# Kernel tuning notes

Measured on AMD Instinct MI355X. Metric: run time of the kernel, lower is better.

The kernel has to match this reference:

```python
import jax, jax.numpy as jnp
import numpy as np

N_NODES = 100000


def gcn_conv(x, src, dst, W, b, n_nodes):
    """PyG GCNConv: out = D^{-1/2} (A + I) D^{-1/2} (x @ W) + b.
    src/dst are the original (non-self-loop) edges; self loops handled analytically.
    """
    h = x @ W  # [N, out]
    ones = jnp.ones(src.shape[0], dtype=h.dtype)
    # degree including self loop
    deg = jax.ops.segment_sum(ones, dst, num_segments=n_nodes) + 1.0  # [N]
    dinv = jax.lax.rsqrt(deg)
    norm = dinv[src] * dinv[dst]  # [E]
    msg = h[src] * norm[:, None]  # gather + scale
    agg = jax.ops.segment_sum(msg, dst, num_segments=n_nodes)  # scatter-add
    # self-loop contribution: norm = deg^{-1/2} * deg^{-1/2} = 1/deg
    agg = agg + h * (1.0 / deg)[:, None]
    return agg + b


def setup_inputs() -> dict:
    key = jax.random.key(0)
    k1, k2, k3, k4 = jax.random.split(key, 4)
    n, e = N_NODES, 3200000
    x = jax.random.normal(k1, (n, 256), dtype=jnp.float32)
    edge_index = jax.random.randint(k2, (2, e), 0, n, dtype=jnp.int64)
    W1 = jax.random.normal(k3, (256, 64), dtype=jnp.float32) * (1.0 / np.sqrt(256))
    b1 = jnp.zeros((64,), dtype=jnp.float32)
    W2 = jax.random.normal(k4, (64, 4), dtype=jnp.float32) * (1.0 / np.sqrt(64))
    b2 = jnp.zeros((4,), dtype=jnp.float32)
    return {"x": x, "edge_index": edge_index, "W1": W1, "b1": b1, "W2": W2, "b2": b2}


def reference(x, edge_index, W1, b1, W2, b2):
    n = x.shape[0]
    src, dst = edge_index[0], edge_index[1]
    h = gcn_conv(x, src, dst, W1, b1, n)
    h = jax.nn.leaky_relu(h, negative_slope=0.01)  # nn.LeakyReLU default
    # F.dropout in eval mode is identity
    h = gcn_conv(h, src, dst, W2, b2, n)
    return jax.nn.softmax(h, axis=1)
```

## Files before the change

kernel.cpp:

```cpp
#include <hip/hip_runtime.h>
#include <hip/hip_bf16.h>
#include <math.h>


#define NB 512
#define MAXB 512

typedef __attribute__((ext_vector_type(8))) short bf16x8;
typedef __attribute__((ext_vector_type(4))) float f32x4;

__device__ __forceinline__ int edge_val(const void* ep, size_t idx, int is64) {
    if (is64) return (int)(((const long long*)ep)[idx]);
    return ((const int*)ep)[idx];
}

__device__ __forceinline__ unsigned short f2bf(float f) {
    unsigned int u = __float_as_uint(f);
    return (unsigned short)((u + 0x7FFFu + ((u >> 16) & 1u)) >> 16);
}
__device__ __forceinline__ float bf2f(unsigned short b) {
    return __uint_as_float((unsigned int)b << 16);
}

__global__ void detect_width(const unsigned int* __restrict__ ew, int* __restrict__ flag) {
    if (threadIdx.x == 0 && blockIdx.x == 0) {
        int f = 1;
        for (int i = 0; i < 64; ++i)
            if (ew[2 * i + 1] != 0u) { f = 0; break; }
        *flag = f;
    }
}

__global__ __launch_bounds__(256) void hist_pass(
    const void* __restrict__ edges, int E, const int* __restrict__ flagp,
    int* __restrict__ ghist, int B) {
    __shared__ int hist[MAXB];
    const int tid = threadIdx.x;
    for (int i = tid; i < B; i += 256) hist[i] = 0;
    __syncthreads();
    const int is64 = *flagp;
    const int per = (E + NB - 1) / NB;
    const int s0 = blockIdx.x * per;
    const int s1 = min(s0 + per, E);
    for (int i = s0 + tid; i < s1; i += 256) {
        const int d = edge_val(edges, (size_t)E + i, is64);
        atomicAdd(&hist[d >> 8], 1);
    }
    __syncthreads();
    for (int i = tid; i < B; i += 256) ghist[(size_t)blockIdx.x * B + i] = hist[i];
}

__global__ __launch_bounds__(NB) void col_scan(
    const int* __restrict__ ghist, int* __restrict__ goff,
    int* __restrict__ bsum, int B) {
    __shared__ int sm[NB];
    const int tid = threadIdx.x;
    const int b = blockIdx.x;
    const int v = ghist[(size_t)tid * B + b];
    sm[tid] = v;
    __syncthreads();
    for (int off = 1; off < NB; off <<= 1) {
        int val = (tid >= off) ? sm[tid - off] : 0;
        __syncthreads();
        sm[tid] += val;
        __syncthreads();
    }
    goff[(size_t)tid * B + b] = sm[tid] - v;
    if (tid == NB - 1) bsum[b] = sm[tid];
}

__global__ __launch_bounds__(512) void base_scan(
    const int* __restrict__ bsum, int* __restrict__ bbase,
    int* __restrict__ row_ptr, int B, int n, int E) {
    __shared__ int sm[512];
    const int tid = threadIdx.x;
    const int v = (tid < B) ? bsum[tid] : 0;
    sm[tid] = v;
    __syncthreads();
    for (int off = 1; off < 512; off <<= 1) {
        int val = (tid >= off) ? sm[tid - off] : 0;
        __syncthreads();
        sm[tid] += val;
        __syncthreads();
    }
    if (tid < B) bbase[tid] = sm[tid] - v;
    if (tid == 0) { bbase[B] = E; row_ptr[n] = E; }
}

__global__ __launch_bounds__(256) void scatter_pass(
    const void* __restrict__ edges, int E, const int* __restrict__ flagp,
    const int* __restrict__ goff, const int* __restrict__ bbase,
    unsigned int* __restrict__ ebuf, int B) {
    __shared__ int off[MAXB];
    const int tid = threadIdx.x;
    for (int i = tid; i < B; i += 256) off[i] = bbase[i] + goff[(size_t)blockIdx.x * B + i];
    __syncthreads();
    const int is64 = *flagp;
    const int per = (E + NB - 1) / NB;
    const int s0 = blockIdx.x * per;
    const int s1 = min(s0 + per, E);
    for (int i = s0 + tid; i < s1; i += 256) {
        const int d = edge_val(edges, (size_t)E + i, is64);
        const int s = edge_val(edges, (size_t)i, is64);
        const int pos = atomicAdd(&off[d >> 8], 1);
        ebuf[pos] = ((unsigned int)s << 8) | (unsigned int)(d & 255);
    }
}

__global__ __launch_bounds__(512) void bucket_csr(
    const unsigned int* __restrict__ ebuf, const int* __restrict__ bbase,
    int* __restrict__ row_ptr, float* __restrict__ dinv,
    int* __restrict__ col_src, int n) {
    __shared__ int hist[256];
    __shared__ int scn[256];
    __shared__ int fill[256];
    const int tid = threadIdx.x;
    const int b = blockIdx.x;
    if (tid < 256) hist[tid] = 0;
    __syncthreads();
    const int base = bbase[b];
    const int m = bbase[b + 1] - base;
    const unsigned int* eb = ebuf + base;
    for (int i = tid; i < m; i += 512) atomicAdd(&hist[eb[i] & 255u], 1);
    __syncthreads();
    if (tid < 256) scn[tid] = hist[tid];
    __syncthreads();
    for (int off = 1; off < 256; off <<= 1) {
        int val = 0;
        if (tid < 256 && tid >= off) val = scn[tid - off];
        __syncthreads();
        if (tid < 256) scn[tid] += val;
        __syncthreads();
    }
    if (tid < 256) {
        const int excl = scn[tid] - hist[tid];
        fill[tid] = excl;
        const int v = b * 256 + tid;
        if (v < n) {
            row_ptr[v] = base + excl;
            dinv[v] = rsqrtf((float)hist[tid] + 1.0f);
        }
    }
    __syncthreads();
    for (int i = tid; i < m; i += 512) {
        const unsigned int e = eb[i];
        const int p = atomicAdd(&fill[e & 255u], 1);
        col_src[base + p] = (int)(e >> 8);
    }
}

__global__ __launch_bounds__(256) void gemm1_kernel(
    const float* __restrict__ x, const float* __restrict__ W1,
    const float* __restrict__ dinv, unsigned short* __restrict__ hs1b, int n) {
    __shared__ unsigned short wt[64 * 264];
    const int tid = threadIdx.x;
    for (int i = tid; i < 4096; i += 256) {
        const int k = i >> 4;
        const int c0 = (i & 15) * 4;
        const float4 w = *((const float4*)W1 + i);
        wt[(c0 + 0) * 264 + k] = f2bf(w.x);
        wt[(c0 + 1) * 264 + k] = f2bf(w.y);
        wt[(c0 + 2) * 264 + k] = f2bf(w.z);
        wt[(c0 + 3) * 264 + k] = f2bf(w.w);
    }
    __syncthreads();

    const int lane = tid & 63;
    const int wid = tid >> 6;
    const int row0 = blockIdx.x * 64 + wid * 16;
    const int rr = lane & 15;
    const int kh = lane >> 4;

    union FragU { bf16x8 v; unsigned short u[8]; };
    bf16x8 af[8];
    {
        int r = row0 + rr;
        if (r >= n) r = n - 1;
        const float* xr = x + (size_t)r * 256 + kh * 8;
#pragma unroll
        for (int ks = 0; ks < 8; ++ks) {
            const float4 p0 = *(const float4*)(xr + ks * 32);
            const float4 p1 = *(const float4*)(xr + ks * 32 + 4);
            FragU f;
            f.u[0] = f2bf(p0.x); f.u[1] = f2bf(p0.y);
            f.u[2] = f2bf(p0.z); f.u[3] = f2bf(p0.w);
            f.u[4] = f2bf(p1.x); f.u[5] = f2bf(p1.y);
            f.u[6] = f2bf(p1.z); f.u[7] = f2bf(p1.w);
            af[ks] = f.v;
        }
    }
    f32x4 acc[4];
#pragma unroll
    for (int ct = 0; ct < 4; ++ct) acc[ct] = (f32x4){0.f, 0.f, 0.f, 0.f};
#pragma unroll
    for (int ct = 0; ct < 4; ++ct) {
        const unsigned short* wcol = wt + (ct * 16 + rr) * 264 + kh * 8;
#pragma unroll
        for (int ks = 0; ks < 8; ++ks) {
            const bf16x8 bf = *(const bf16x8*)(wcol + ks * 32);
            acc[ct] = __builtin_amdgcn_mfma_f32_16x16x32_bf16(af[ks], bf, acc[ct], 0, 0, 0);
        }
    }
#pragma unroll
    for (int j = 0; j < 4; ++j) {
        const int gr = row0 + kh * 4 + j;
        if (gr < n) {
            const float dv = dinv[gr];
#pragma unroll
            for (int ct = 0; ct < 4; ++ct)
                hs1b[(size_t)gr * 64 + ct * 16 + rr] = f2bf(acc[ct][j] * dv);
        }
    }
}

__global__ __launch_bounds__(256) void agg1_kernel(
    const int* __restrict__ row_ptr, const int* __restrict__ col_src,
    const unsigned short* __restrict__ hs1b, const float* __restrict__ dinv,
    const float* __restrict__ b1, const float* __restrict__ W2,
    float* __restrict__ hs2, int n) {
    const int lane = threadIdx.x & 63;
    int v = blockIdx.x * 4 + (threadIdx.x >> 6);
    v = __builtin_amdgcn_readfirstlane(v);
    if (v >= n) return;
    const int g = lane >> 4;
    const int q = lane & 15;
    const int rs = row_ptr[v];
    const int re = row_ptr[v + 1];
    float a0 = 0.f, a1 = 0.f, a2 = 0.f, a3 = 0.f;
    int e = rs;
    for (; e + 16 <= re; e += 16) {
        const int cs = col_src[e + q];
        const int s0 = __shfl(cs, 0 + g);
        const int s1 = __shfl(cs, 4 + g);
        const int s2 = __shfl(cs, 8 + g);
        const int s3 = __shfl(cs, 12 + g);
        const ushort4 r0 = *((const ushort4*)(hs1b + (size_t)s0 * 64) + q);
        const ushort4 r1 = *((const ushort4*)(hs1b + (size_t)s1 * 64) + q);
        const ushort4 r2 = *((const ushort4*)(hs1b + (size_t)s2 * 64) + q);
        const ushort4 r3 = *((const ushort4*)(hs1b + (size_t)s3 * 64) + q);
        a0 += bf2f(r0.x) + bf2f(r1.x) + bf2f(r2.x) + bf2f(r3.x);
        a1 += bf2f(r0.y) + bf2f(r1.y) + bf2f(r2.y) + bf2f(r3.y);
        a2 += bf2f(r0.z) + bf2f(r1.z) + bf2f(r2.z) + bf2f(r3.z);
        a3 += bf2f(r0.w) + bf2f(r1.w) + bf2f(r2.w) + bf2f(r3.w);
    }
    for (; e < re; e += 4) {
        if (e + g < re) {
            const int s = col_src[e + g];
            const ushort4 r = *((const ushort4*)(hs1b + (size_t)s * 64) + q);
            a0 += bf2f(r.x); a1 += bf2f(r.y); a2 += bf2f(r.z); a3 += bf2f(r.w);
        }
    }
    a0 += __shfl_xor(a0, 16); a1 += __shfl_xor(a1, 16);
    a2 += __shfl_xor(a2, 16); a3 += __shfl_xor(a3, 16);
    a0 += __shfl_xor(a0, 32); a1 += __shfl_xor(a1, 32);
    a2 += __shfl_xor(a2, 32); a3 += __shfl_xor(a3, 32);
    const ushort4 sr = *((const ushort4*)(hs1b + (size_t)v * 64) + q);
    const float dv = dinv[v];
    const float4 bb = *((const float4*)b1 + q);
    float4 res;
    res.x = dv * (a0 + bf2f(sr.x)) + bb.x;
    res.y = dv * (a1 + bf2f(sr.y)) + bb.y;
    res.z = dv * (a2 + bf2f(sr.z)) + bb.z;
    res.w = dv * (a3 + bf2f(sr.w)) + bb.w;
    res.x = res.x > 0.f ? res.x : 0.01f * res.x;
    res.y = res.y > 0.f ? res.y : 0.01f * res.y;
    res.z = res.z > 0.f ? res.z : 0.01f * res.z;
    res.w = res.w > 0.f ? res.w : 0.01f * res.w;
    const float4* W2v = (const float4*)W2;
    const float4 w0 = W2v[q * 4 + 0], w1 = W2v[q * 4 + 1];
    const float4 w2 = W2v[q * 4 + 2], w3 = W2v[q * 4 + 3];
    float4 p;
    p.x = res.x * w0.x + res.y * w1.x + res.z * w2.x + res.w * w3.x;
    p.y = res.x * w0.y + res.y * w1.y + res.z * w2.y + res.w * w3.y;
    p.z = res.x * w0.z + res.y * w1.z + res.z * w2.z + res.w * w3.z;
    p.w = res.x * w0.w + res.y * w1.w + res.z * w2.w + res.w * w3.w;
#pragma unroll
    for (int s = 1; s < 16; s <<= 1) {
        p.x += __shfl_xor(p.x, s); p.y += __shfl_xor(p.y, s);
        p.z += __shfl_xor(p.z, s); p.w += __shfl_xor(p.w, s);
    }
    if (lane == 0) {
        float4 o; o.x = p.x * dv; o.y = p.y * dv; o.z = p.z * dv; o.w = p.w * dv;
        *(float4*)(hs2 + (size_t)v * 4) = o;
    }
}

__global__ __launch_bounds__(256) void agg2_kernel(
    const int* __restrict__ row_ptr, const int* __restrict__ col_src,
    const float* __restrict__ hs2, const float* __restrict__ dinv,
    const float* __restrict__ b2, float* __restrict__ out, int n) {
    const int lane = threadIdx.x & 63;
    int v = blockIdx.x * 4 + (threadIdx.x >> 6);
    v = __builtin_amdgcn_readfirstlane(v);
    if (v >= n) return;
    const int c = lane & 3;
    const int ei = lane >> 2;
    const int rs = row_ptr[v];
    const int re = row_ptr[v + 1];
    float acc = 0.f;
    for (int e0 = rs; e0 < re; e0 += 16) {
        const int e = e0 + ei;
        if (e < re) {
            const int s = col_src[e];
            acc += hs2[(size_t)s * 4 + c];
        }
    }
    acc += __shfl_xor(acc, 4);
    acc += __shfl_xor(acc, 8);
    acc += __shfl_xor(acc, 16);
    acc += __shfl_xor(acc, 32);
    const float val = dinv[v] * (acc + hs2[(size_t)v * 4 + c]) + b2[c];
    float m = fmaxf(val, __shfl_xor(val, 1));
    m = fmaxf(m, __shfl_xor(m, 2));
    const float ex = __expf(val - m);
    float s = ex + __shfl_xor(ex, 1);
    s += __shfl_xor(s, 2);
    if (lane < 4) out[(size_t)v * 4 + c] = ex / s;
}

extern "C" void kernel_launch(void* const* d_in, const int* in_sizes, int n_in,
                              void* d_out, int out_size, void* d_ws, size_t ws_size,
                              hipStream_t stream) {
    const float* x  = (const float*)d_in[0];
    const void*  ei = d_in[1];
    const float* W1 = (const float*)d_in[2];
    const float* b1 = (const float*)d_in[3];
    const float* W2 = (const float*)d_in[4];
    const float* b2 = (const float*)d_in[5];
    const int n = in_sizes[0] / 256;
    const int E = in_sizes[1] / 2;
    const int B = (n + 255) / 256;

    char* ws = (char*)d_ws;
    size_t off = 0;
    auto alloc = [&](size_t bytes) -> void* {
        void* p = ws + off;
        off += (bytes + 255) & ~(size_t)255;
        return p;
    };
    int*   flag    = (int*)alloc(sizeof(int) * 64);
    int*   ghist   = (int*)alloc(sizeof(int) * (size_t)NB * B);
    int*   goff    = (int*)alloc(sizeof(int) * (size_t)NB * B);
    int*   bsum    = (int*)alloc(sizeof(int) * B);
    int*   bbase   = (int*)alloc(sizeof(int) * (B + 1));
    int*   row_ptr = (int*)alloc(sizeof(int) * (n + 1));
    int*   col_src = (int*)alloc(sizeof(int) * (size_t)E);
    float* dinv    = (float*)alloc(sizeof(float) * n);
    unsigned short* hs1b = (unsigned short*)alloc(sizeof(unsigned short) * (size_t)n * 64);
    float* hs2     = (float*)alloc(sizeof(float) * (size_t)n * 4);
    unsigned int* ebuf = (unsigned int*)alloc(sizeof(unsigned int) * (size_t)E);
    (void)n_in; (void)out_size; (void)ws_size;

    detect_width<<<1, 64, 0, stream>>>((const unsigned int*)ei, flag);
    hist_pass<<<NB, 256, 0, stream>>>(ei, E, flag, ghist, B);
    col_scan<<<B, NB, 0, stream>>>(ghist, goff, bsum, B);
    base_scan<<<1, 512, 0, stream>>>(bsum, bbase, row_ptr, B, n, E);
    scatter_pass<<<NB, 256, 0, stream>>>(ei, E, flag, goff, bbase, ebuf, B);
    bucket_csr<<<B, 512, 0, stream>>>(ebuf, bbase, row_ptr, dinv, col_src, n);
    gemm1_kernel<<<(n + 63) / 64, 256, 0, stream>>>(x, W1, dinv, hs1b, n);
    agg1_kernel<<<(n + 3) / 4, 256, 0, stream>>>(row_ptr, col_src, hs1b, dinv, b1, W2, hs2, n);
    agg2_kernel<<<(n + 3) / 4, 256, 0, stream>>>(row_ptr, col_src, hs2, dinv, b2, (float*)d_out, n);
}
```

Measured before the change: 211.2 us.

## Stage scatter in LDS for coalesced bucket writes; unroll agg1 gather to 32 edges

The scatter pass now sorts each block's chunk of edges by bucket in shared memory, using a local prefix scan over the per-block histogram. It then writes each bucket's run to global memory contiguously with wave-wide copies, replacing scattered single-word global writes. The block size rises to 512 threads, and a fallback keeps the old path when a chunk exceeds the LDS buffer. Separately, agg1 processes 32 edges per iteration with two accumulator sets, putting more independent gathers in flight. This costs more LDS and registers, which may lower occupancy.

New measurement: 210.5 us. No clear change (-0.3%).

```diff
diff --git a/kernel.cpp b/kernel.cpp
--- a/kernel.cpp
+++ b/kernel.cpp
@@ -5,6 +5,7 @@
 
 #define NB 512
 #define MAXB 512
+#define SCHUNK 6400
 
 typedef __attribute__((ext_vector_type(8))) short bf16x8;
 typedef __attribute__((ext_vector_type(4))) float f32x4;
@@ -87,23 +88,61 @@
     if (tid == 0) { bbase[B] = E; row_ptr[n] = E; }
 }
 
-__global__ __launch_bounds__(256) void scatter_pass(
+__global__ __launch_bounds__(512) void scatter_pass(
     const void* __restrict__ edges, int E, const int* __restrict__ flagp,
-    const int* __restrict__ goff, const int* __restrict__ bbase,
-    unsigned int* __restrict__ ebuf, int B) {
-    __shared__ int off[MAXB];
-    const int tid = threadIdx.x;
-    for (int i = tid; i < B; i += 256) off[i] = bbase[i] + goff[(size_t)blockIdx.x * B + i];
-    __syncthreads();
+    const int* __restrict__ ghist, const int* __restrict__ goff,
+    const int* __restrict__ bbase, unsigned int* __restrict__ ebuf, int B) {
+    __shared__ unsigned int buf[SCHUNK];
+    __shared__ int lb[MAXB];
+    __shared__ int lf[MAXB];
+    __shared__ int sm[MAXB];
+    const int tid = threadIdx.x;
+    const int blk = blockIdx.x;
     const int is64 = *flagp;
     const int per = (E + NB - 1) / NB;
-    const int s0 = blockIdx.x * per;
+    const int s0 = blk * per;
     const int s1 = min(s0 + per, E);
-    for (int i = s0 + tid; i < s1; i += 256) {
-        const int d = edge_val(edges, (size_t)E + i, is64);
-        const int s = edge_val(edges, (size_t)i, is64);
-        const int pos = atomicAdd(&off[d >> 8], 1);
-        ebuf[pos] = ((unsigned int)s << 8) | (unsigned int)(d & 255);
+
+    if (per <= SCHUNK) {
+        const int c = (tid < B) ? ghist[(size_t)blk * B + tid] : 0;
+        sm[tid] = c;
+        __syncthreads();
+        for (int off = 1; off < MAXB; off <<= 1) {
+            int val = (tid >= off) ? sm[tid - off] : 0;
+            __syncthreads();
+            sm[tid] += val;
+            __syncthreads();
+        }
+        if (tid < B) { lb[tid] = sm[tid] - c; lf[tid] = sm[tid] - c; }
+        __syncthreads();
+        for (int i = s0 + tid; i < s1; i += 512) {
+            const int d = edge_val(edges, (size_t)E + i, is64);
+            const int s = edge_val(edges, (size_t)i, is64);
+            const unsigned int val = ((unsigned int)s << 8) | (unsigned int)(d & 255);
+            const int pos = atomicAdd(&lf[d >> 8], 1);
+            buf[pos] = val;
+        }
+        __syncthreads();
+        const int lane = tid & 63;
+        const int wv = tid >> 6;
+        for (int b = wv; b < B; b += 8) {
+            const int lo = lb[b];
+            const int cnt = lf[b] - lo;
+            if (cnt > 0) {
+                unsigned int* dst = ebuf + bbase[b] + goff[(size_t)blk * B + b];
+                for (int k = lane; k < cnt; k += 64) dst[k] = buf[lo + k];
+            }
+        }
+    } else {
+        for (int i = tid; i < B; i += 512)
+            lf[i] = bbase[i] + goff[(size_t)blk * B + i];
+        __syncthreads();
+        for (int i = s0 + tid; i < s1; i += 512) {
+            const int d = edge_val(edges, (size_t)E + i, is64);
+            const int s = edge_val(edges, (size_t)i, is64);
+            const int pos = atomicAdd(&lf[d >> 8], 1);
+            ebuf[pos] = ((unsigned int)s << 8) | (unsigned int)(d & 255);
+        }
     }
 }
 
@@ -227,7 +266,32 @@
     const int rs = row_ptr[v];
     const int re = row_ptr[v + 1];
     float a0 = 0.f, a1 = 0.f, a2 = 0.f, a3 = 0.f;
+    float c0 = 0.f, c1 = 0.f, c2 = 0.f, c3 = 0.f;
     int e = rs;
+    for (; e + 32 <= re; e += 32) {
+        const int cs = col_src[e + (lane & 31)];
+        const int s0 = __shfl(cs, 0 + g),  s1 = __shfl(cs, 4 + g);
+        const int s2 = __shfl(cs, 8 + g),  s3 = __shfl(cs, 12 + g);
+        const int s4 = __shfl(cs, 16 + g), s5 = __shfl(cs, 20 + g);
+        const int s6 = __shfl(cs, 24 + g), s7 = __shfl(cs, 28 + g);
+        const ushort4 r0 = *((const ushort4*)(hs1b + (size_t)s0 * 64) + q);
+        const ushort4 r1 = *((const ushort4*)(hs1b + (size_t)s1 * 64) + q);
+        const ushort4 r2 = *((const ushort4*)(hs1b + (size_t)s2 * 64) + q);
+        const ushort4 r3 = *((const ushort4*)(hs1b + (size_t)s3 * 64) + q);
+        const ushort4 r4 = *((const ushort4*)(hs1b + (size_t)s4 * 64) + q);
+        const ushort4 r5 = *((const ushort4*)(hs1b + (size_t)s5 * 64) + q);
+        const ushort4 r6 = *((const ushort4*)(hs1b + (size_t)s6 * 64) + q);
+        const ushort4 r7 = *((const ushort4*)(hs1b + (size_t)s7 * 64) + q);
+        a0 += bf2f(r0.x) + bf2f(r1.x) + bf2f(r2.x) + bf2f(r3.x);
+        a1 += bf2f(r0.y) + bf2f(r1.y) + bf2f(r2.y) + bf2f(r3.y);
+        a2 += bf2f(r0.z) + bf2f(r1.z) + bf2f(r2.z) + bf2f(r3.z);
+        a3 += bf2f(r0.w) + bf2f(r1.w) + bf2f(r2.w) + bf2f(r3.w);
+        c0 += bf2f(r4.x) + bf2f(r5.x) + bf2f(r6.x) + bf2f(r7.x);
+        c1 += bf2f(r4.y) + bf2f(r5.y) + bf2f(r6.y) + bf2f(r7.y);
+        c2 += bf2f(r4.z) + bf2f(r5.z) + bf2f(r6.z) + bf2f(r7.z);
+        c3 += bf2f(r4.w) + bf2f(r5.w) + bf2f(r6.w) + bf2f(r7.w);
+    }
+    a0 += c0; a1 += c1; a2 += c2; a3 += c3;
     for (; e + 16 <= re; e += 16) {
         const int cs = col_src[e + q];
         const int s0 = __shfl(cs, 0 + g);
@@ -355,7 +419,7 @@
     hist_pass<<<NB, 256, 0, stream>>>(ei, E, flag, ghist, B);
     col_scan<<<B, NB, 0, stream>>>(ghist, goff, bsum, B);
     base_scan<<<1, 512, 0, stream>>>(bsum, bbase, row_ptr, B, n, E);
-    scatter_pass<<<NB, 256, 0, stream>>>(ei, E, flag, goff, bbase, ebuf, B);
+    scatter_pass<<<NB, 512, 0, stream>>>(ei, E, flag, ghist, goff, bbase, ebuf, B);
     bucket_csr<<<B, 512, 0, stream>>>(ebuf, bbase, row_ptr, dinv, col_src, n);
     gemm1_kernel<<<(n + 63) / 64, 256, 0, stream>>>(x, W1, dinv, hs1b, n);
     agg1_kernel<<<(n + 3) / 4, 256, 0, stream>>>(row_ptr, col_src, hs1b, dinv, b1, W2, hs2, n);
```
